# Optimization experiments

Hardware: AMD Instinct MI355X
Metric: run time of the kernel (lower is better)

## Reference

```python
import jax, jax.numpy as jnp
import numpy as np

S, B, IN, H, DFF, OUT, L, NHEAD, WINDOW = 2048, 4, 64, 1024, 1024, 64, 3, 4, 4
EPS = 1e-5


def _layer_norm(x, scale, bias):
    m = jnp.mean(x, axis=-1, keepdims=True)
    v = jnp.var(x, axis=-1, keepdims=True)
    return (x - m) * jax.lax.rsqrt(v + EPS) * scale + bias


def setup_inputs() -> dict:
    key = jax.random.key(0)
    ks = jax.random.split(key, 12)
    s = 0.02
    return {
        "src": jax.random.normal(ks[0], (S, B, IN), dtype=jnp.float32),
        "Wenc": jax.random.normal(ks[1], (H, IN), dtype=jnp.float32) * s,
        "benc": jnp.zeros((H,), jnp.float32),
        "Wqkv": jax.random.normal(ks[2], (L, 3 * H, H), dtype=jnp.float32) * s,
        "bqkv": jnp.zeros((L, 3 * H), jnp.float32),
        "Wo": jax.random.normal(ks[3], (L, H, H), dtype=jnp.float32) * s,
        "bo": jnp.zeros((L, H), jnp.float32),
        "W1": jax.random.normal(ks[4], (L, DFF, H), dtype=jnp.float32) * s,
        "b1": jnp.zeros((L, DFF), jnp.float32),
        "W2": jax.random.normal(ks[5], (L, H, DFF), dtype=jnp.float32) * s,
        "b2": jnp.zeros((L, H), jnp.float32),
        "ln1_s": jnp.ones((L, H), jnp.float32),
        "ln1_b": jnp.zeros((L, H), jnp.float32),
        "ln2_s": jnp.ones((L, H), jnp.float32),
        "ln2_b": jnp.zeros((L, H), jnp.float32),
        "Wout": jax.random.normal(ks[6], (OUT, H), dtype=jnp.float32) * s,
        "bout": jnp.zeros((OUT,), jnp.float32),
    }


def _banded_mask(sz):
    # triu(1) masked + lower-band (j < i-4) masked => allowed: i-4 <= j <= i
    i = jnp.arange(sz)[:, None]
    j = jnp.arange(sz)[None, :]
    allowed = (j <= i) & (j >= i - WINDOW)
    return jnp.where(allowed, 0.0, -1e9).astype(jnp.float32)


def reference(src, Wenc, benc, Wqkv, bqkv, Wo, bo, W1, b1, W2, b2,
              ln1_s, ln1_b, ln2_s, ln2_b, Wout, bout):
    dh = H // NHEAD
    mask = _banded_mask(src.shape[0])  # [S, S]
    x = src @ Wenc.T + benc  # [S, B, H]  (NOTE: pos_encoder is never applied in the source)

    def layer(x, p):
        Wqkv_, bqkv_, Wo_, bo_, W1_, b1_, W2_, b2_, s1, g1, s2, g2 = p
        qkv = x @ Wqkv_.T + bqkv_  # [S, B, 3H]
        q, k, v = jnp.split(qkv, 3, axis=-1)
        sS, sB = x.shape[0], x.shape[1]
        q = q.reshape(sS, sB, NHEAD, dh)
        k = k.reshape(sS, sB, NHEAD, dh)
        v = v.reshape(sS, sB, NHEAD, dh)
        scores = jnp.einsum('sbhd,tbhd->bhst', q, k) / jnp.sqrt(jnp.float32(dh))
        scores = scores + mask  # broadcast over [b, h]
        attn = jax.nn.softmax(scores, axis=-1)
        ctx = jnp.einsum('bhst,tbhd->sbhd', attn, v).reshape(sS, sB, H)
        attn_out = ctx @ Wo_.T + bo_
        x = _layer_norm(x + attn_out, s1, g1)  # post-norm (PyTorch default)
        ff = jax.nn.relu(x @ W1_.T + b1_) @ W2_.T + b2_
        x = _layer_norm(x + ff, s2, g2)
        return x, None

    x, _ = jax.lax.scan(layer, x, (Wqkv, bqkv, Wo, bo, W1, b1, W2, b2,
                                   ln1_s, ln1_b, ln2_s, ln2_b))
    return x @ Wout.T + bout  # [S, B, OUT]
```

## Files before the change

kernel.cpp:

```cpp
#include <hip/hip_runtime.h>
#include <hip/hip_bf16.h>

#define S_LEN   2048
#define BATCH   4
#define IN_DIM  64
#define H_DIM   1024
#define DFF_DIM 1024
#define OUT_DIM 64
#define NLAYER  3
#define NHEADS  4
#define DHEAD   256
#define WIN     4
#define ROWS    (S_LEN*BATCH)
#define QKV_LD  (3*H_DIM)


typedef __bf16 bf16x8 __attribute__((ext_vector_type(8)));
typedef float  f32x4  __attribute__((ext_vector_type(4)));

__device__ __forceinline__ float bfbits2f(unsigned int u) {
  union { unsigned int i; float f; } c; c.i = u << 16; return c.f;
}
__device__ __forceinline__ unsigned short f2bfbits(float f) {
  __hip_bfloat16 h = __float2bfloat16(f);
  return __builtin_bit_cast(unsigned short, h);
}

__device__ __forceinline__ void g2l16(const void* g, void* l) {
  __builtin_amdgcn_global_load_lds((__attribute__((address_space(1))) void*)g,
                                   (__attribute__((address_space(3))) void*)l,
                                   16, 0, 0);
}

struct CvtSeg { const float* src; __hip_bfloat16* dst; int n4; };

__global__ __launch_bounds__(256)
void cvt_all_k(CvtSeg s0, CvtSeg s1, CvtSeg s2, CvtSeg s3,
               CvtSeg s4, CvtSeg s5, CvtSeg s6)
{
  int i = blockIdx.x * 256 + threadIdx.x;
  CvtSeg seg;
  if      (i < s0.n4) { seg = s0; }
  else if ((i -= s0.n4) < s1.n4) { seg = s1; }
  else if ((i -= s1.n4) < s2.n4) { seg = s2; }
  else if ((i -= s2.n4) < s3.n4) { seg = s3; }
  else if ((i -= s3.n4) < s4.n4) { seg = s4; }
  else if ((i -= s4.n4) < s5.n4) { seg = s5; }
  else if ((i -= s5.n4) < s6.n4) { seg = s6; }
  else return;
  float4 v = *(const float4*)(seg.src + (size_t)i * 4);
  uint2 o;
  o.x = (unsigned)f2bfbits(v.x) | ((unsigned)f2bfbits(v.y) << 16);
  o.y = (unsigned)f2bfbits(v.z) | ((unsigned)f2bfbits(v.w) << 16);
  *(uint2*)(seg.dst + (size_t)i * 4) = o;
}

template<int RELU, int OUTF32, int ADDRES>
__global__ __launch_bounds__(256, 2)
void gemm_bt(const __hip_bfloat16* __restrict__ A, int lda,
             const __hip_bfloat16* __restrict__ B,
             const float* __restrict__ bias,
             void* __restrict__ Cp, int ldc,
             const __hip_bfloat16* __restrict__ R, int ldr,
             int M, int N, int K)
{
  __shared__ __align__(16) __hip_bfloat16 As[128 * 64];
  __shared__ __align__(16) __hip_bfloat16 Bs[128 * 64];

  const int tid  = threadIdx.x;
  const int lane = tid & 63;
  const int wave = tid >> 6;
  const int quad = lane >> 4;
  const int l16  = lane & 15;

  const int gx  = gridDim.x;
  const int lin = blockIdx.y * gx + blockIdx.x;
  const int gsz = 4 * gx;
  const int mt  = (lin / gsz) * 4 + (lin & 3);
  const int nt  = (lin % gsz) >> 2;
  const int m0 = mt * 128;
  const int n0 = nt * 128;

  const int wr = (wave >> 1) * 64;
  const int wc = (wave & 1) * 64;

  int arow[4], acol[4], brow[4];
#pragma unroll
  for (int s = 0; s < 4; s++) {
    const int p = tid + (s << 8);
    arow[s] = p >> 3;
    acol[s] = ((p & 7) ^ ((p >> 3) & 7)) * 8;
    brow[s] = min(n0 + arow[s], N - 1);
  }

  f32x4 acc[4][4] = {};
  const int nk = K >> 6;

  for (int t = 0; t < nk; ++t) {
    const int k0 = t << 6;
#pragma unroll
    for (int s = 0; s < 4; s++) {
      const int lo = (wave * 64 + (s << 8)) * 8;
      g2l16(A + (size_t)(m0 + arow[s]) * lda + k0 + acol[s], &As[lo]);
      g2l16(B + (size_t)brow[s] * K + k0 + acol[s], &Bs[lo]);
    }
    __syncthreads();

#pragma unroll
    for (int kh = 0; kh < 2; kh++) {
      bf16x8 af[4], bfr[4];
#pragma unroll
      for (int i = 0; i < 4; i++) {
        const int row = wr + i * 16 + l16;
        const int c   = (kh * 4 + quad) ^ (row & 7);
        af[i] = *(const bf16x8*)&As[row * 64 + c * 8];
      }
#pragma unroll
      for (int j = 0; j < 4; j++) {
        const int row = wc + j * 16 + l16;
        const int c   = (kh * 4 + quad) ^ (row & 7);
        bfr[j] = *(const bf16x8*)&Bs[row * 64 + c * 8];
      }
#pragma unroll
      for (int i = 0; i < 4; i++)
#pragma unroll
        for (int j = 0; j < 4; j++)
          acc[i][j] = __builtin_amdgcn_mfma_f32_16x16x32_bf16(af[i], bfr[j], acc[i][j], 0, 0, 0);
    }
    __syncthreads();
  }

#pragma unroll
  for (int j = 0; j < 4; j++) {
    int col = n0 + wc + j * 16 + l16;
    if (col < N) {
      float bv = bias[col];
#pragma unroll
      for (int i = 0; i < 4; i++) {
        int row = m0 + wr + i * 16 + quad * 4;
#pragma unroll
        for (int r = 0; r < 4; r++) {
          float v = acc[i][j][r] + bv;
          if (RELU) v = fmaxf(v, 0.f);
          if (ADDRES) v += __bfloat162float(R[(size_t)(row + r) * ldr + col]);
          if (OUTF32) ((float*)Cp)[(size_t)(row + r) * ldc + col] = v;
          else ((__hip_bfloat16*)Cp)[(size_t)(row + r) * ldc + col] = __float2bfloat16(v);
        }
      }
    }
  }
}

#define R3_SA(BUF, KO)                                                        \
  do {                                                                        \
    __hip_bfloat16* d_ = &lds[BUF][0];                                        \
    _Pragma("unroll") for (int s_ = 0; s_ < 2; s_++)                          \
      g2l16(Ab + (size_t)arow[s_] * lda + (KO) + acol[s_],                    \
            d_ + (((wave << 6) + (s_ << 9)) << 3));                           \
  } while (0)
#define R3_SB0(BUF, KO)                                                       \
  do {                                                                        \
    __hip_bfloat16* d_ = &lds[BUF][8192];                                     \
    _Pragma("unroll") for (int s_ = 0; s_ < 2; s_++)                          \
      g2l16(Bb + (size_t)arow[s_] * K + (KO) + acol[s_],                      \
            d_ + (((wave << 6) + (s_ << 9)) << 3));                           \
  } while (0)
#define R3_SB1(BUF, KO)                                                       \
  do {                                                                        \
    __hip_bfloat16* d_ = &lds[BUF][8192];                                     \
    _Pragma("unroll") for (int s_ = 2; s_ < 4; s_++)                          \
      g2l16(Bb + (size_t)arow[s_] * K + (KO) + acol[s_],                      \
            d_ + (((wave << 6) + (s_ << 9)) << 3));                           \
  } while (0)

#define R3_PH(BUF, KS, STAGE_STMT, WAIT_STMT)                                 \
  do {                                                                        \
    bf16x8 af[4], bq[4];                                                      \
    const __hip_bfloat16* As_ = &lds[BUF][0];                                 \
    const __hip_bfloat16* Bs_ = &lds[BUF][8192];                              \
    _Pragma("unroll") for (int im = 0; im < 4; im++) {                        \
      const int r_ = wm * 64 + im * 16 + l16;                                 \
      af[im] = *(const bf16x8*)&As_[r_ * 64 + ((((KS)*4 + quad) ^ (r_ & 7)) << 3)]; \
    }                                                                         \
    _Pragma("unroll") for (int jn = 0; jn < 4; jn++) {                        \
      const int r_ = wn * 64 + jn * 16 + l16;                                 \
      bq[jn] = *(const bf16x8*)&Bs_[r_ * 64 + ((((KS)*4 + quad) ^ (r_ & 7)) << 3)]; \
    }                                                                         \
    STAGE_STMT;                                                               \
    WAIT_STMT;                                                                \
    __builtin_amdgcn_s_barrier();                                             \
    asm volatile("s_waitcnt lgkmcnt(0)" ::: "memory");                        \
    __builtin_amdgcn_sched_barrier(0);                                        \
    __builtin_amdgcn_s_setprio(1);                                            \
    _Pragma("unroll") for (int im = 0; im < 4; im++)                          \
      _Pragma("unroll") for (int jn = 0; jn < 4; jn++)                        \
        acc[im][jn] = __builtin_amdgcn_mfma_f32_16x16x32_bf16(                \
            af[im], bq[jn], acc[im][jn], 0, 0, 0);                            \
    __builtin_amdgcn_s_setprio(0);                                            \
    __builtin_amdgcn_s_barrier();                                             \
  } while (0)

template<int RELU, int ADDRES>
__global__ __launch_bounds__(512, 1)
void gemm3r_bt(const __hip_bfloat16* __restrict__ A, int lda,
               const __hip_bfloat16* __restrict__ B,
               const float* __restrict__ bias,
               __hip_bfloat16* __restrict__ C, int ldc,
               const __hip_bfloat16* __restrict__ Rr, int ldr,
               int K)
{
  __shared__ __align__(16) __hip_bfloat16 lds[3][24576];

  const int tid  = threadIdx.x;
  const int lane = tid & 63;
  const int wave = tid >> 6;
  const int quad = lane >> 4;
  const int l16  = lane & 15;
  const int wm   = wave >> 2;
  const int wn   = wave & 3;

  const int gx  = gridDim.x;
  const int lin = blockIdx.y * gx + blockIdx.x;
  const int gsz = 4 * gx;
  const int mt  = (lin / gsz) * 4 + (lin & 3);
  const int nt  = (lin % gsz) >> 2;
  const int m0 = mt * 128;
  const int n0 = nt * 256;

  const __hip_bfloat16* Ab = A + (size_t)m0 * lda;
  const __hip_bfloat16* Bb = B + (size_t)n0 * K;

  int arow[4], acol[4];
#pragma unroll
  for (int s = 0; s < 4; s++) {
    const int p = tid + (s << 9);
    arow[s] = p >> 3;
    acol[s] = ((p & 7) ^ (arow[s] & 7)) << 3;
  }

  f32x4 acc[4][4] = {};
  const int NK = K >> 6;

  R3_SA(0, 0);  R3_SB0(0, 0);  R3_SB1(0, 0);
  R3_SA(1, 64); R3_SB0(1, 64); R3_SB1(1, 64);
  asm volatile("s_waitcnt vmcnt(6)" ::: "memory");
  __builtin_amdgcn_s_barrier();

  for (int t = 0; t < NK; ++t) {
    const int r  = t % 3;
    const int rn = (t + 2) % 3;
    const int k2 = (t + 2) << 6;
    const bool pf = (t + 2) < NK;

    R3_PH(r, 0,
          if (pf) { R3_SA(rn, k2); R3_SB0(rn, k2); }, );
    R3_PH(r, 1,
          if (pf) { R3_SB1(rn, k2); },
          if (pf) { asm volatile("s_waitcnt vmcnt(6)" ::: "memory"); }
          else    { asm volatile("s_waitcnt vmcnt(0)" ::: "memory"); });
  }

#pragma unroll
  for (int jn = 0; jn < 4; jn++) {
    const int col = n0 + wn * 64 + jn * 16 + l16;
    const float bv = bias[col];
#pragma unroll
    for (int im = 0; im < 4; im++) {
      const int row0 = m0 + wm * 64 + im * 16 + quad * 4;
      const f32x4 a = acc[im][jn];
#pragma unroll
      for (int rr = 0; rr < 4; rr++) {
        float v = a[rr] + bv;
        if (RELU) v = fmaxf(v, 0.f);
        if (ADDRES) v += __bfloat162float(Rr[(size_t)(row0 + rr) * ldr + col]);
        C[(size_t)(row0 + rr) * ldc + col] = __float2bfloat16(v);
      }
    }
  }
}

__global__ __launch_bounds__(256)
void attn_k(__hip_bfloat16* __restrict__ qkv)
{
  const int gw   = (blockIdx.x << 2) + (threadIdx.x >> 6);
  const int lane = threadIdx.x & 63;
  const int h = gw & (NHEADS - 1);
  const int b = (gw >> 2) & (BATCH - 1);
  const int s = gw >> 4;
  const size_t hoff = (size_t)h * DHEAD + (lane << 2);

  float q0, q1, q2, q3;
  {
    uint2 t = *(const uint2*)(qkv + (size_t)(s * BATCH + b) * QKV_LD + hoff);
    q0 = bfbits2f(t.x & 0xffff); q1 = bfbits2f(t.x >> 16);
    q2 = bfbits2f(t.y & 0xffff); q3 = bfbits2f(t.y >> 16);
  }

  float sc[WIN + 1];
#pragma unroll
  for (int jj = 0; jj <= WIN; jj++) {
    int j = s - WIN + jj;
    float v = -1e30f;
    if (j >= 0) {
      uint2 t = *(const uint2*)(qkv + (size_t)(j * BATCH + b) * QKV_LD + H_DIM + hoff);
      float p = q0 * bfbits2f(t.x & 0xffff) + q1 * bfbits2f(t.x >> 16)
              + q2 * bfbits2f(t.y & 0xffff) + q3 * bfbits2f(t.y >> 16);
#pragma unroll
      for (int o = 32; o; o >>= 1) p += __shfl_xor(p, o);
      v = p * 0.0625f;
    }
    sc[jj] = v;
  }

  float mx = sc[0];
#pragma unroll
  for (int jj = 1; jj <= WIN; jj++) mx = fmaxf(mx, sc[jj]);
  float p[WIN + 1], den = 0.f;
#pragma unroll
  for (int jj = 0; jj <= WIN; jj++) { p[jj] = __expf(sc[jj] - mx); den += p[jj]; }

  float a0 = 0.f, a1 = 0.f, a2 = 0.f, a3 = 0.f;
#pragma unroll
  for (int jj = 0; jj <= WIN; jj++) {
    int j = s - WIN + jj;
    if (j >= 0) {
      uint2 t = *(const uint2*)(qkv + (size_t)(j * BATCH + b) * QKV_LD + 2 * H_DIM + hoff);
      a0 += p[jj] * bfbits2f(t.x & 0xffff); a1 += p[jj] * bfbits2f(t.x >> 16);
      a2 += p[jj] * bfbits2f(t.y & 0xffff); a3 += p[jj] * bfbits2f(t.y >> 16);
    }
  }
  float rl = 1.f / den;
  uint2 o;
  o.x = (unsigned)f2bfbits(a0 * rl) | ((unsigned)f2bfbits(a1 * rl) << 16);
  o.y = (unsigned)f2bfbits(a2 * rl) | ((unsigned)f2bfbits(a3 * rl) << 16);
  *(uint2*)(qkv + (size_t)(s * BATCH + b) * QKV_LD + hoff) = o;
}

__global__ __launch_bounds__(256)
void ln_k(const __hip_bfloat16* __restrict__ y, int ys,
          const float* __restrict__ g, const float* __restrict__ be,
          __hip_bfloat16* __restrict__ xout)
{
  const int row  = blockIdx.x * 4 + (threadIdx.x >> 6);
  const int lane = threadIdx.x & 63;
  const int e0   = lane * 16;
  const __hip_bfloat16* yp = y + (size_t)row * ys + e0;

  uint2 v[4];
  *(uint4*)&v[0] = *(const uint4*)yp;
  *(uint4*)&v[2] = *(const uint4*)(yp + 8);
  float t[16];
#pragma unroll
  for (int k = 0; k < 4; k++) {
    t[k * 4 + 0] = bfbits2f(v[k].x & 0xffff);
    t[k * 4 + 1] = bfbits2f(v[k].x >> 16);
    t[k * 4 + 2] = bfbits2f(v[k].y & 0xffff);
    t[k * 4 + 3] = bfbits2f(v[k].y >> 16);
  }
  float s = 0.f, ss = 0.f;
#pragma unroll
  for (int k = 0; k < 16; k++) { s += t[k]; ss += t[k] * t[k]; }
#pragma unroll
  for (int o = 32; o; o >>= 1) { s += __shfl_xor(s, o); ss += __shfl_xor(ss, o); }

  const float inv  = 1.f / (float)H_DIM;
  const float mean = s * inv;
  const float var  = ss * inv - mean * mean;
  const float rstd = rsqrtf(var + 1e-5f);

  float4 gv[4], bv[4];
#pragma unroll
  for (int k = 0; k < 4; k++) {
    gv[k] = *(const float4*)(g + e0 + k * 4);
    bv[k] = *(const float4*)(be + e0 + k * 4);
  }
  uint2 ob[4];
#pragma unroll
  for (int k = 0; k < 4; k++) {
    float o0 = (t[k*4+0] - mean) * rstd * gv[k].x + bv[k].x;
    float o1 = (t[k*4+1] - mean) * rstd * gv[k].y + bv[k].y;
    float o2 = (t[k*4+2] - mean) * rstd * gv[k].z + bv[k].z;
    float o3 = (t[k*4+3] - mean) * rstd * gv[k].w + bv[k].w;
    ob[k].x = (unsigned)f2bfbits(o0) | ((unsigned)f2bfbits(o1) << 16);
    ob[k].y = (unsigned)f2bfbits(o2) | ((unsigned)f2bfbits(o3) << 16);
  }
  __hip_bfloat16* xp = xout + (size_t)row * H_DIM + e0;
  *(uint4*)xp       = *(const uint4*)&ob[0];
  *(uint4*)(xp + 8) = *(const uint4*)&ob[2];
}

extern "C" void kernel_launch(void* const* d_in, const int* in_sizes, int n_in,
                              void* d_out, int out_size, void* d_ws, size_t ws_size,
                              hipStream_t stream) {
  const float* src   = (const float*)d_in[0];
  const float* Wenc  = (const float*)d_in[1];
  const float* benc  = (const float*)d_in[2];
  const float* Wqkv  = (const float*)d_in[3];
  const float* bqkv  = (const float*)d_in[4];
  const float* Wo    = (const float*)d_in[5];
  const float* bo    = (const float*)d_in[6];
  const float* W1    = (const float*)d_in[7];
  const float* b1    = (const float*)d_in[8];
  const float* W2    = (const float*)d_in[9];
  const float* b2    = (const float*)d_in[10];
  const float* ln1s  = (const float*)d_in[11];
  const float* ln1b  = (const float*)d_in[12];
  const float* ln2s  = (const float*)d_in[13];
  const float* ln2b  = (const float*)d_in[14];
  const float* Wout  = (const float*)d_in[15];
  const float* bout  = (const float*)d_in[16];

  char* ws = (char*)d_ws;
  __hip_bfloat16* WB   = (__hip_bfloat16*)ws;
  __hip_bfloat16* srcb = WB;
  __hip_bfloat16* wenc = WB + 524288;
  __hip_bfloat16* wqkv = WB + 589824;
  __hip_bfloat16* wo   = WB + 10027008;
  __hip_bfloat16* w1   = WB + 13172736;
  __hip_bfloat16* w2   = WB + 16318464;
  __hip_bfloat16* wout = WB + 19464192;
  __hip_bfloat16* xb  = (__hip_bfloat16*)(ws + (size_t)40 * 1048576);
  __hip_bfloat16* qkv = (__hip_bfloat16*)(ws + (size_t)56 * 1048576);
  __hip_bfloat16* ctxp = qkv;
  __hip_bfloat16* ybuf = qkv + H_DIM;
  __hip_bfloat16* hbuf = qkv + 2 * H_DIM;

  const dim3 blk(256);
  const dim3 blk512(512);

  {
    CvtSeg s0{src,  srcb, 524288 / 4};
    CvtSeg s1{Wenc, wenc, 65536 / 4};
    CvtSeg s2{Wqkv, wqkv, 9437184 / 4};
    CvtSeg s3{Wo,   wo,   3145728 / 4};
    CvtSeg s4{W1,   w1,   3145728 / 4};
    CvtSeg s5{W2,   w2,   3145728 / 4};
    CvtSeg s6{Wout, wout, 65536 / 4};
    const int tot4 = (524288 + 65536 + 9437184 + 3 * 3145728 + 65536) / 4;
    cvt_all_k<<<dim3((tot4 + 255) / 256), blk, 0, stream>>>(s0, s1, s2, s3, s4, s5, s6);
  }

  gemm_bt<0, 0, 0><<<dim3(H_DIM / 128, ROWS / 128), blk, 0, stream>>>(
      srcb, IN_DIM, wenc, benc, xb, H_DIM, nullptr, 0, ROWS, H_DIM, IN_DIM);

  for (int l = 0; l < NLAYER; l++) {
    gemm3r_bt<0, 0><<<dim3(QKV_LD / 256, ROWS / 128), blk512, 0, stream>>>(
        xb, H_DIM, wqkv + (size_t)l * QKV_LD * H_DIM, bqkv + l * QKV_LD,
        qkv, QKV_LD, nullptr, 0, H_DIM);
    attn_k<<<dim3(ROWS * NHEADS / 4), blk, 0, stream>>>(qkv);
    gemm3r_bt<0, 1><<<dim3(H_DIM / 256, ROWS / 128), blk512, 0, stream>>>(
        ctxp, QKV_LD, wo + (size_t)l * H_DIM * H_DIM, bo + l * H_DIM,
        ybuf, QKV_LD, xb, H_DIM, H_DIM);
    ln_k<<<dim3(ROWS / 4), blk, 0, stream>>>(ybuf, QKV_LD, ln1s + l * H_DIM, ln1b + l * H_DIM, xb);
    gemm3r_bt<1, 0><<<dim3(DFF_DIM / 256, ROWS / 128), blk512, 0, stream>>>(
        xb, H_DIM, w1 + (size_t)l * DFF_DIM * H_DIM, b1 + l * DFF_DIM,
        hbuf, QKV_LD, nullptr, 0, H_DIM);
    gemm3r_bt<0, 1><<<dim3(H_DIM / 256, ROWS / 128), blk512, 0, stream>>>(
        hbuf, QKV_LD, w2 + (size_t)l * H_DIM * DFF_DIM, b2 + l * H_DIM,
        ybuf, QKV_LD, xb, H_DIM, DFF_DIM);
    ln_k<<<dim3(ROWS / 4), blk, 0, stream>>>(ybuf, QKV_LD, ln2s + l * H_DIM, ln2b + l * H_DIM, xb);
  }

  gemm_bt<0, 1, 0><<<dim3(1, ROWS / 128), blk, 0, stream>>>(
      xb, H_DIM, wout, bout, d_out, OUT_DIM, nullptr, 0, ROWS, OUT_DIM, H_DIM);
}
```

Before: 697.7 us.

## Restructure GEMM into 8-phase double-buffered pipeline with split LDS halves

Replaces the triple-buffered two-phase-per-k-tile GEMM with a double-buffered kernel that runs eight phases per 128-wide k pair. Each phase does a 2x2 quadrant of MFMAs over the full 64-wide k step, with LDS fragment reads and global-to-LDS staging interleaved in finer pieces. The goal is to hide global load latency and LDS reads behind MFMA work while cutting LDS use from three buffers to two. In exchange it adds more barriers per k-step, and the prefetch distance is shorter, which could expose memory latency.

Measured after the change: 699.1 us. No clear change (+0.2%).

```diff
diff --git a/kernel.cpp b/kernel.cpp
--- a/kernel.cpp
+++ b/kernel.cpp
@@ -151,65 +151,74 @@
   }
 }
 
-#define R3_SA(BUF, KO)                                                        \
-  do {                                                                        \
-    __hip_bfloat16* d_ = &lds[BUF][0];                                        \
-    _Pragma("unroll") for (int s_ = 0; s_ < 2; s_++)                          \
-      g2l16(Ab + (size_t)arow[s_] * lda + (KO) + acol[s_],                    \
-            d_ + (((wave << 6) + (s_ << 9)) << 3));                           \
-  } while (0)
-#define R3_SB0(BUF, KO)                                                       \
-  do {                                                                        \
-    __hip_bfloat16* d_ = &lds[BUF][8192];                                     \
-    _Pragma("unroll") for (int s_ = 0; s_ < 2; s_++)                          \
-      g2l16(Bb + (size_t)arow[s_] * K + (KO) + acol[s_],                      \
-            d_ + (((wave << 6) + (s_ << 9)) << 3));                           \
-  } while (0)
-#define R3_SB1(BUF, KO)                                                       \
-  do {                                                                        \
-    __hip_bfloat16* d_ = &lds[BUF][8192];                                     \
-    _Pragma("unroll") for (int s_ = 2; s_ < 4; s_++)                          \
-      g2l16(Bb + (size_t)arow[s_] * K + (KO) + acol[s_],                      \
-            d_ + (((wave << 6) + (s_ << 9)) << 3));                           \
-  } while (0)
-
-#define R3_PH(BUF, KS, STAGE_STMT, WAIT_STMT)                                 \
-  do {                                                                        \
-    bf16x8 af[4], bq[4];                                                      \
-    const __hip_bfloat16* As_ = &lds[BUF][0];                                 \
-    const __hip_bfloat16* Bs_ = &lds[BUF][8192];                              \
-    _Pragma("unroll") for (int im = 0; im < 4; im++) {                        \
-      const int r_ = wm * 64 + im * 16 + l16;                                 \
-      af[im] = *(const bf16x8*)&As_[r_ * 64 + ((((KS)*4 + quad) ^ (r_ & 7)) << 3)]; \
+#define ST_A(BUF, H, KO)                                                      \
+  g2l16(Ab + (size_t)((H) * 64 + sarow) * lda + (KO) + sacol,                 \
+        &lds[BUF][(H) << 12] + (tid << 3))
+#define ST_B(BUF, H, KO)                                                      \
+  do {                                                                        \
+    g2l16(Bb + (size_t)((H) * 128 + sbrow) * K + (KO) + sbcol,                \
+          &lds[BUF][8192 + ((H) << 13)] + (tid << 3));                        \
+    g2l16(Bb + (size_t)((H) * 128 + sbrow + 64) * K + (KO) + sbcol,           \
+          &lds[BUF][8192 + ((H) << 13)] + ((tid + 512) << 3));                \
+  } while (0)
+
+#define RD_AF(ASL, FRB)                                                       \
+  do {                                                                        \
+    _Pragma("unroll") for (int j_ = 0; j_ < 2; j_++) {                        \
+      const int r_ = ((FRB) + j_) * 16 + l16;                                 \
+      const int x_ = r_ & 7;                                                  \
+      af[j_][0] = *(const bf16x8*)&(ASL)[r_ * 64 + ((quad ^ x_) << 3)];       \
+      af[j_][1] = *(const bf16x8*)&(ASL)[r_ * 64 + (((4 + quad) ^ x_) << 3)]; \
     }                                                                         \
-    _Pragma("unroll") for (int jn = 0; jn < 4; jn++) {                        \
-      const int r_ = wn * 64 + jn * 16 + l16;                                 \
-      bq[jn] = *(const bf16x8*)&Bs_[r_ * 64 + ((((KS)*4 + quad) ^ (r_ & 7)) << 3)]; \
+  } while (0)
+#define RD_BQ(BSL, FCB)                                                       \
+  do {                                                                        \
+    _Pragma("unroll") for (int j_ = 0; j_ < 2; j_++) {                        \
+      const int r_ = brow_base + ((FCB) + j_) * 16 + l16;                     \
+      const int x_ = r_ & 7;                                                  \
+      bq[(FCB) + j_][0] = *(const bf16x8*)&(BSL)[r_ * 64 + ((quad ^ x_) << 3)]; \
+      bq[(FCB) + j_][1] = *(const bf16x8*)&(BSL)[r_ * 64 + (((4 + quad) ^ x_) << 3)]; \
     }                                                                         \
-    STAGE_STMT;                                                               \
-    WAIT_STMT;                                                                \
+  } while (0)
+#define MM(FRB, FCB)                                                          \
+  do {                                                                        \
+    _Pragma("unroll") for (int ks_ = 0; ks_ < 2; ks_++)                       \
+      _Pragma("unroll") for (int i_ = 0; i_ < 2; i_++)                        \
+        _Pragma("unroll") for (int j_ = 0; j_ < 2; j_++)                      \
+          acc[(FRB) + i_][(FCB) + j_] =                                       \
+              __builtin_amdgcn_mfma_f32_16x16x32_bf16(                        \
+                  af[i_][ks_], bq[(FCB) + j_][ks_],                           \
+                  acc[(FRB) + i_][(FCB) + j_], 0, 0, 0);                      \
+  } while (0)
+
+#define PH8(READS, STAGE, WAIT, MFMA)                                         \
+  do {                                                                        \
+    READS; STAGE; WAIT;                                                       \
     __builtin_amdgcn_s_barrier();                                             \
     asm volatile("s_waitcnt lgkmcnt(0)" ::: "memory");                        \
     __builtin_amdgcn_sched_barrier(0);                                        \
     __builtin_amdgcn_s_setprio(1);                                            \
-    _Pragma("unroll") for (int im = 0; im < 4; im++)                          \
-      _Pragma("unroll") for (int jn = 0; jn < 4; jn++)                        \
-        acc[im][jn] = __builtin_amdgcn_mfma_f32_16x16x32_bf16(                \
-            af[im], bq[jn], acc[im][jn], 0, 0, 0);                            \
+    MFMA;                                                                     \
     __builtin_amdgcn_s_setprio(0);                                            \
     __builtin_amdgcn_s_barrier();                                             \
   } while (0)
 
+#define W4CNT                                                                 \
+  do {                                                                        \
+    if (pf) { asm volatile("s_waitcnt vmcnt(4)" ::: "memory"); }              \
+    else    { asm volatile("s_waitcnt vmcnt(0)" ::: "memory"); }              \
+  } while (0)
+
 template<int RELU, int ADDRES>
 __global__ __launch_bounds__(512, 1)
-void gemm3r_bt(const __hip_bfloat16* __restrict__ A, int lda,
-               const __hip_bfloat16* __restrict__ B,
-               const float* __restrict__ bias,
-               __hip_bfloat16* __restrict__ C, int ldc,
-               const __hip_bfloat16* __restrict__ Rr, int ldr,
-               int K)
+void gemm8_bt(const __hip_bfloat16* __restrict__ A, int lda,
+              const __hip_bfloat16* __restrict__ B,
+              const float* __restrict__ bias,
+              __hip_bfloat16* __restrict__ C, int ldc,
+              const __hip_bfloat16* __restrict__ Rr, int ldr,
+              int K)
 {
-  __shared__ __align__(16) __hip_bfloat16 lds[3][24576];
+  __shared__ __align__(16) __hip_bfloat16 lds[2][24576];
 
   const int tid  = threadIdx.x;
   const int lane = tid & 63;
@@ -218,6 +227,8 @@
   const int l16  = lane & 15;
   const int wm   = wave >> 2;
   const int wn   = wave & 3;
+  const int bh   = wn >> 1;
+  const int brow_base = (wn & 1) * 64;
 
   const int gx  = gridDim.x;
   const int lin = blockIdx.y * gx + blockIdx.x;
@@ -230,34 +241,41 @@
   const __hip_bfloat16* Ab = A + (size_t)m0 * lda;
   const __hip_bfloat16* Bb = B + (size_t)n0 * K;
 
-  int arow[4], acol[4];
-#pragma unroll
-  for (int s = 0; s < 4; s++) {
-    const int p = tid + (s << 9);
-    arow[s] = p >> 3;
-    acol[s] = ((p & 7) ^ (arow[s] & 7)) << 3;
-  }
+  const int sarow = tid >> 3;
+  const int sacol = ((tid & 7) ^ (sarow & 7)) << 3;
+  const int sbrow = sarow;
+  const int sbcol = sacol;
+
+  const __hip_bfloat16* As0 = &lds[0][wm << 12];
+  const __hip_bfloat16* As1 = &lds[1][wm << 12];
+  const __hip_bfloat16* Bs0 = &lds[0][8192 + (bh << 13)];
+  const __hip_bfloat16* Bs1 = &lds[1][8192 + (bh << 13)];
 
   f32x4 acc[4][4] = {};
-  const int NK = K >> 6;
-
-  R3_SA(0, 0);  R3_SB0(0, 0);  R3_SB1(0, 0);
-  R3_SA(1, 64); R3_SB0(1, 64); R3_SB1(1, 64);
-  asm volatile("s_waitcnt vmcnt(6)" ::: "memory");
+  bf16x8 af[2][2], bq[4][2];
+
+  const int NI = K >> 7;
+
+  ST_A(0, 0, 0); ST_A(0, 1, 0);
+  ST_B(0, 0, 0); ST_B(0, 1, 0);
+  ST_B(1, 0, 64); ST_B(1, 1, 64);
+  asm volatile("s_waitcnt vmcnt(4)" ::: "memory");
   __builtin_amdgcn_s_barrier();
 
-  for (int t = 0; t < NK; ++t) {
-    const int r  = t % 3;
-    const int rn = (t + 2) % 3;
-    const int k2 = (t + 2) << 6;
-    const bool pf = (t + 2) < NK;
-
-    R3_PH(r, 0,
-          if (pf) { R3_SA(rn, k2); R3_SB0(rn, k2); }, );
-    R3_PH(r, 1,
-          if (pf) { R3_SB1(rn, k2); },
-          if (pf) { asm volatile("s_waitcnt vmcnt(6)" ::: "memory"); }
-          else    { asm volatile("s_waitcnt vmcnt(0)" ::: "memory"); });
+  for (int i = 0; i < NI; ++i) {
+    const int k1 = (i << 7) + 64;
+    const int k2 = k1 + 64;
+    const int k3 = k1 + 128;
+    const bool pf = (i + 1) < NI;
+
+    PH8(RD_AF(As0, 0); RD_BQ(Bs0, 0),  ST_A(1, 0, k1),              , MM(0, 0));
+    PH8(RD_BQ(Bs0, 2),                 ST_A(1, 1, k1),              , MM(0, 2));
+    PH8(RD_AF(As0, 2),                 if (pf) ST_B(0, 0, k2),      , MM(2, 0));
+    PH8(                             , if (pf) ST_B(0, 1, k2), W4CNT, MM(2, 2));
+    PH8(RD_AF(As1, 0); RD_BQ(Bs1, 0),  if (pf) ST_A(0, 0, k2),      , MM(0, 0));
+    PH8(RD_BQ(Bs1, 2),                 if (pf) ST_A(0, 1, k2),      , MM(0, 2));
+    PH8(RD_AF(As1, 2),                 if (pf) ST_B(1, 0, k3),      , MM(2, 0));
+    PH8(                             , if (pf) ST_B(1, 1, k3), W4CNT, MM(2, 2));
   }
 
 #pragma unroll
@@ -444,18 +462,18 @@
       srcb, IN_DIM, wenc, benc, xb, H_DIM, nullptr, 0, ROWS, H_DIM, IN_DIM);
 
   for (int l = 0; l < NLAYER; l++) {
-    gemm3r_bt<0, 0><<<dim3(QKV_LD / 256, ROWS / 128), blk512, 0, stream>>>(
+    gemm8_bt<0, 0><<<dim3(QKV_LD / 256, ROWS / 128), blk512, 0, stream>>>(
         xb, H_DIM, wqkv + (size_t)l * QKV_LD * H_DIM, bqkv + l * QKV_LD,
         qkv, QKV_LD, nullptr, 0, H_DIM);
     attn_k<<<dim3(ROWS * NHEADS / 4), blk, 0, stream>>>(qkv);
-    gemm3r_bt<0, 1><<<dim3(H_DIM / 256, ROWS / 128), blk512, 0, stream>>>(
+    gemm8_bt<0, 1><<<dim3(H_DIM / 256, ROWS / 128), blk512, 0, stream>>>(
         ctxp, QKV_LD, wo + (size_t)l * H_DIM * H_DIM, bo + l * H_DIM,
         ybuf, QKV_LD, xb, H_DIM, H_DIM);
     ln_k<<<dim3(ROWS / 4), blk, 0, stream>>>(ybuf, QKV_LD, ln1s + l * H_DIM, ln1b + l * H_DIM, xb);
-    gemm3r_bt<1, 0><<<dim3(DFF_DIM / 256, ROWS / 128), blk512, 0, stream>>>(
+    gemm8_bt<1, 0><<<dim3(DFF_DIM / 256, ROWS / 128), blk512, 0, stream>>>(
         xb, H_DIM, w1 + (size_t)l * DFF_DIM * H_DIM, b1 + l * DFF_DIM,
         hbuf, QKV_LD, nullptr, 0, H_DIM);
-    gemm3r_bt<0, 1><<<dim3(H_DIM / 256, ROWS / 128), blk512, 0, stream>>>(
+    gemm8_bt<0, 1><<<dim3(H_DIM / 256, ROWS / 128), blk512, 0, stream>>>(
         hbuf, QKV_LD, w2 + (size_t)l * H_DIM * DFF_DIM, b2 + l * H_DIM,
         ybuf, QKV_LD, xb, H_DIM, DFF_DIM);
     ln_k<<<dim3(ROWS / 4), blk, 0, stream>>>(ybuf, QKV_LD, ln2s + l * H_DIM, ln2b + l * H_DIM, xb);
```
